# Optimization experiments

Hardware: AMD Instinct MI355X
Metric: run time of the kernel (lower is better)

Reference implementation:

```python
import jax, jax.numpy as jnp
import numpy as np


def setup_inputs() -> dict:
    key = jax.random.key(0)
    ks = jax.random.split(key, 7)
    N, C, sy, sx = 1024, 384, 7, 7
    Dm, Dc = 64, 64
    Dg = C + Dm + Dc  # 512, must match f_t_global
    return {
        "f_t_global": jax.random.normal(ks[0], (N, Dg), dtype=jnp.float32),
        "x_t_local": jax.random.normal(ks[1], (N, C, sy, sx), dtype=jnp.float32),
        "x_t_prev_local": jax.random.normal(ks[2], (N, C, sy, sx), dtype=jnp.float32),
        "m_t": jax.random.normal(ks[3], (N, Dm), dtype=jnp.float32),
        "m_t_prev": jax.random.normal(ks[4], (N, Dm), dtype=jnp.float32),
        "c_t": jax.random.normal(ks[5], (N, Dc), dtype=jnp.float32),
        "c_t_prev": jax.random.normal(ks[6], (N, Dc), dtype=jnp.float32),
    }


def _join(loc, m, c):
    # loc: [S, N, C]; m: [N, Dm]; c: [N, Dc] -> [S, N, C+Dm+Dc]
    S, N, _ = loc.shape
    mc = jnp.concatenate([m, c], axis=-1)  # [N, Dm+Dc]
    mc = jnp.broadcast_to(mc[None], (S, N, mc.shape[-1]))
    return jnp.concatenate([loc, mc], axis=-1)


def _mean_ce_diag(logits):
    # logits: [S, N, N]; labels = arange(N) for every s -> mean over s of CE
    logp = jax.nn.log_softmax(logits, axis=-1)
    diag = jnp.diagonal(logp, axis1=1, axis2=2)  # [S, N]
    return -jnp.mean(diag)  # mean over N (per-step CE) and over S (the /(sx*sy))


def reference(f_t_global, x_t_local, x_t_prev_local, m_t, m_t_prev, c_t, c_t_prev):
    N, C, sy, sx = x_t_prev_local.shape
    S = sy * sx
    # [N,C,sy,sx] -> [S,N,C] (spatial locations batched)
    prev = x_t_prev_local.reshape(N, C, S).transpose(2, 0, 1)
    cur = x_t_local.reshape(N, C, S).transpose(2, 0, 1)
    pos = _join(prev, m_t_prev, c_t_prev)   # [S, N, D]
    # loss1: global features vs per-location previous positives
    logits1 = jnp.einsum('id,sjd->sij', f_t_global, pos)  # [S, N, N]
    loss1 = _mean_ce_diag(logits1)
    # loss2: per-location current predictions vs previous positives
    pred2 = _join(cur, m_t, c_t)            # [S, N, D]
    logits2 = jnp.einsum('sid,sjd->sij', pred2, pos)
    loss2 = _mean_ce_diag(logits2)
    loss = loss1 + loss2
    return (loss, x_t_prev_local, x_t_local)
```

## Files before the change

### kernel.cpp

```cpp
#include <hip/hip_runtime.h>
#include <hip/hip_bf16.h>

typedef __attribute__((ext_vector_type(8))) __bf16 bf16x8;
typedef __attribute__((ext_vector_type(4))) float  f32x4;

#define SDIM 49
#define NDIM 1024
#define CDIM 384
#define DDIM 512
#define DMC  64
#define SCALE (1.0f/(SDIM*NDIM))
#define SLOT 65536

__device__ __forceinline__ void gload16(const void* g, void* l) {
    __builtin_amdgcn_global_load_lds((const __attribute__((address_space(1))) void*)g,
                                     (__attribute__((address_space(3))) void*)l, 16, 0, 0);
}

__global__ __launch_bounds__(512) void pack_copy_kernel(
    const float* __restrict__ xloc, const float* __restrict__ mv,
    const float* __restrict__ cv,   __hip_bfloat16* __restrict__ dst,
    float* __restrict__ cpy)
{
    const int j = blockIdx.x;
    const int d = threadIdx.x;
    float vals[SDIM];
    if (d < CDIM) {
        const float* p = xloc + ((size_t)j * CDIM + d) * SDIM;
        #pragma unroll
        for (int s = 0; s < SDIM; ++s) vals[s] = p[s];
    } else if (d < CDIM + DMC) {
        float v = mv[j * DMC + (d - CDIM)];
        #pragma unroll
        for (int s = 0; s < SDIM; ++s) vals[s] = v;
    } else {
        float v = cv[j * DMC + (d - CDIM - DMC)];
        #pragma unroll
        for (int s = 0; s < SDIM; ++s) vals[s] = v;
    }
    #pragma unroll
    for (int s = 0; s < SDIM; ++s)
        dst[((size_t)s * NDIM + j) * DDIM + d] = __float2bfloat16(vals[s]);

    const float* src = xloc + (size_t)j * CDIM * SDIM;
    float* dcp = cpy + (size_t)j * CDIM * SDIM;
    for (int i = threadIdx.x; i < CDIM * SDIM; i += 512) dcp[i] = src[i];
}

__global__ void fpack_kernel(const float* __restrict__ f,
                             __hip_bfloat16* __restrict__ dst, int n)
{
    int i = blockIdx.x * blockDim.x + threadIdx.x;
    if (i < n) dst[i] = __float2bfloat16(f[i]);
}

__global__ __launch_bounds__(512, 2) void loss_kernel(
    const __hip_bfloat16* __restrict__ Fm,
    const __hip_bfloat16* __restrict__ Km,
    const __hip_bfloat16* __restrict__ Qm,
    float2* __restrict__ part,
    float* __restrict__ out)
{
    extern __shared__ __attribute__((aligned(16))) char sm[];

    const int bid = blockIdx.x;
    const int gid = (bid & 7) * 196 + (bid >> 3);
    const int s   = gid >> 5;
    const int rem = gid & 31;
    const int kb  = rem >> 3;
    const int qb  = rem & 7;

    const int tid  = threadIdx.x;
    const int lane = tid & 63;
    const int w    = tid >> 6;
    const int l15  = lane & 15;
    const int l4   = lane >> 4;
    const int wk   = w >> 2;
    const int wq   = w & 3;

    const char* Ag = (const char*)Km + ((size_t)s * NDIM + (size_t)kb * 256) * 1024;
    const char* Bg = (qb < 4)
        ? ((const char*)Fm + (size_t)qb * 256 * 1024)
        : ((const char*)Qm + ((size_t)s * NDIM + (size_t)(qb - 4) * 256) * 1024);

    const int trow = tid >> 3;
    const int scol = (((tid & 7) ^ ((tid >> 3) & 7)) << 4);

    #define STAGE(T) do {                                                     \
        char* sb_ = sm + (size_t)((T) & 1) * SLOT;                            \
        const size_t ko_ = (size_t)(T) * 128;                                 \
        _Pragma("unroll")                                                     \
        for (int c = 0; c < 4; ++c) {                                         \
            gload16(Ag + (size_t)(c * 64 + trow) * 1024 + ko_ + scol,         \
                    sb_ + c * 8192 + tid * 16);                               \
            gload16(Bg + (size_t)(c * 64 + trow) * 1024 + ko_ + scol,         \
                    sb_ + 32768 + c * 8192 + tid * 16);                       \
        }                                                                     \
    } while (0)

    const unsigned xo   = (unsigned)((l15 & 7) << 4);
    const unsigned arow = (unsigned)((wk * 128 + l15) * 128);
    const unsigned brow = 32768u + (unsigned)((wq * 64 + l15) * 128);

    f32x4 acc[8][4];
    #pragma unroll
    for (int a = 0; a < 8; ++a)
        #pragma unroll
        for (int b = 0; b < 4; ++b) acc[a][b] = f32x4{0.f, 0.f, 0.f, 0.f};

    #define COMPUTE(T) do {                                                   \
        const char* sb_ = sm + (size_t)((T) & 1) * SLOT;                      \
        _Pragma("unroll")                                                     \
        for (int kc = 0; kc < 2; ++kc) {                                      \
            const unsigned col = ((unsigned)(kc * 64 + l4 * 16)) ^ xo;        \
            bf16x8 bfr[4], afr[8];                                            \
            _Pragma("unroll")                                                 \
            for (int b = 0; b < 4; ++b)                                       \
                bfr[b] = *(const bf16x8*)(sb_ + brow + b * 2048 + col);       \
            _Pragma("unroll")                                                 \
            for (int a = 0; a < 8; ++a)                                       \
                afr[a] = *(const bf16x8*)(sb_ + arow + a * 2048 + col);       \
            _Pragma("unroll")                                                 \
            for (int a = 0; a < 8; ++a)                                       \
                _Pragma("unroll")                                             \
                for (int b = 0; b < 4; ++b)                                   \
                    acc[a][b] = __builtin_amdgcn_mfma_f32_16x16x32_bf16(      \
                        afr[a], bfr[b], acc[a][b], 0, 0, 0);                  \
        }                                                                     \
    } while (0)

    STAGE(0);
    for (int t = 0; t < 8; ++t) {
        if (t < 7) {
            STAGE(t + 1);
            asm volatile("s_waitcnt vmcnt(8)" ::: "memory");
        } else {
            asm volatile("s_waitcnt vmcnt(0)" ::: "memory");
        }
        __builtin_amdgcn_s_barrier();
        __builtin_amdgcn_s_setprio(1);
        COMPUTE(t);
        __builtin_amdgcn_s_setprio(0);
        asm volatile("" ::: "memory");
        __builtin_amdgcn_s_barrier();
    }

    float q_m[4], q_s[4];
    #pragma unroll
    for (int b = 0; b < 4; ++b) {
        float m = -3.0e38f;
        #pragma unroll
        for (int a = 0; a < 8; ++a)
            #pragma unroll
            for (int r = 0; r < 4; ++r) m = fmaxf(m, acc[a][b][r]);
        float ss = 0.0f;
        #pragma unroll
        for (int a = 0; a < 8; ++a)
            #pragma unroll
            for (int r = 0; r < 4; ++r) ss += __expf(acc[a][b][r] - m);
        #pragma unroll
        for (int off = 16; off <= 32; off <<= 1) {
            float mo = __shfl_xor(m, off, 64);
            float so = __shfl_xor(ss, off, 64);
            float nm = fmaxf(m, mo);
            ss = ss * __expf(m - nm) + so * __expf(mo - nm);
            m = nm;
        }
        q_m[b] = m; q_s[b] = ss;
    }
    if (lane < 16) {
        const size_t rowb = (size_t)s * 2048 + (size_t)qb * 256 + wq * 64 + lane;
        #pragma unroll
        for (int b = 0; b < 4; ++b)
            part[(rowb + b * 16) * 8 + kb * 2 + wk] = make_float2(q_m[b], q_s[b]);
    }

    if (kb == (qb & 3) && (wq >> 1) == wk) {
        float d = 0.0f;
        const bool lok = (((lane >> 2) & 3) == l4);
        if (wq & 1) {
            #pragma unroll
            for (int b = 0; b < 4; ++b)
                #pragma unroll
                for (int r = 0; r < 4; ++r)
                    if (lok && r == (lane & 3)) d += acc[4 + b][b][r];
        } else {
            #pragma unroll
            for (int b = 0; b < 4; ++b)
                #pragma unroll
                for (int r = 0; r < 4; ++r)
                    if (lok && r == (lane & 3)) d += acc[b][b][r];
        }
        #pragma unroll
        for (int off = 1; off < 64; off <<= 1) d += __shfl_xor(d, off, 64);
        if (lane == 0) atomicAdd(out, -d * SCALE);
    }
    #undef STAGE
    #undef COMPUTE
}

__global__ __launch_bounds__(256) void reduce_kernel(
    const float2* __restrict__ part, float* __restrict__ out)
{
    const int row = blockIdx.x * 256 + threadIdx.x;
    const float2* p = part + (size_t)row * 8;
    float m = -3.0e38f;
    float2 q[8];
    #pragma unroll
    for (int i = 0; i < 8; ++i) { q[i] = p[i]; m = fmaxf(m, q[i].x); }
    float ssum = 0.0f;
    #pragma unroll
    for (int i = 0; i < 8; ++i) ssum += q[i].y * __expf(q[i].x - m);
    float v = m + __logf(ssum);
    #pragma unroll
    for (int off = 1; off < 64; off <<= 1) v += __shfl_xor(v, off, 64);
    __shared__ float red[4];
    const int lane = threadIdx.x & 63, w = threadIdx.x >> 6;
    if (lane == 0) red[w] = v;
    __syncthreads();
    if (threadIdx.x == 0)
        atomicAdd(out, (red[0] + red[1] + red[2] + red[3]) * SCALE);
}

extern "C" void kernel_launch(void* const* d_in, const int* in_sizes, int n_in,
                              void* d_out, int out_size, void* d_ws, size_t ws_size,
                              hipStream_t stream)
{
    (void)in_sizes; (void)n_in; (void)out_size; (void)ws_size;
    const float* f  = (const float*)d_in[0];
    const float* x  = (const float*)d_in[1];
    const float* xp = (const float*)d_in[2];
    const float* mt = (const float*)d_in[3];
    const float* mp = (const float*)d_in[4];
    const float* ct = (const float*)d_in[5];
    const float* cp = (const float*)d_in[6];
    float* out = (float*)d_out;

    char* ws = (char*)d_ws;
    const size_t packBytes = (size_t)SDIM * NDIM * DDIM * 2;
    __hip_bfloat16* Km = (__hip_bfloat16*)ws;
    __hip_bfloat16* Qm = (__hip_bfloat16*)(ws + packBytes);
    __hip_bfloat16* Fm = (__hip_bfloat16*)(ws + 2 * packBytes);
    float2* part = (float2*)(ws + 2 * packBytes + (size_t)NDIM * DDIM * 2);

    hipMemsetAsync(out, 0, sizeof(float), stream);

    const int sz = NDIM * CDIM * SDIM;
    pack_copy_kernel<<<NDIM, 512, 0, stream>>>(xp, mp, cp, Km, out + 1);
    pack_copy_kernel<<<NDIM, 512, 0, stream>>>(x,  mt, ct, Qm, out + 1 + sz);
    fpack_kernel<<<(NDIM * DDIM + 255) / 256, 256, 0, stream>>>(f, Fm, NDIM * DDIM);

    loss_kernel<<<1568, 512, 2 * SLOT, stream>>>(Fm, Km, Qm, part, out);
    reduce_kernel<<<392, 256, 0, stream>>>(part, out);
}
```

Measured before the change: 255.8 us.

## Split K-step into four quadrant phases interleaving LDS reads, prefetch and MFMA

Restructures the GEMM main loop into a four-phase ping-pong schedule. The LDS fragment reads for A and B halves, the global-to-LDS prefetch halves of the next tile, and the MFMA quadrants are interleaved, with barriers separating each phase. The goal is to overlap LDS traffic and global loads with matrix-core work and to lower register pressure by holding only half the fragments at a time. The extra barriers per iteration (eight instead of two) and the full vmcnt(0) wait inside each step could cost more synchronisation time than the overlap saves.

```diff
diff --git a/kernel.cpp b/kernel.cpp
--- a/kernel.cpp
+++ b/kernel.cpp
@@ -86,15 +86,15 @@
     const int trow = tid >> 3;
     const int scol = (((tid & 7) ^ ((tid >> 3) & 7)) << 4);
 
-    #define STAGE(T) do {                                                     \
-        char* sb_ = sm + (size_t)((T) & 1) * SLOT;                            \
+    #define STAGE_HALF(T, H) do {                                             \
+        char* db_ = sm + (size_t)((T) & 1) * SLOT;                            \
         const size_t ko_ = (size_t)(T) * 128;                                 \
         _Pragma("unroll")                                                     \
-        for (int c = 0; c < 4; ++c) {                                         \
+        for (int c = 2 * (H); c < 2 * (H) + 2; ++c) {                         \
             gload16(Ag + (size_t)(c * 64 + trow) * 1024 + ko_ + scol,         \
-                    sb_ + c * 8192 + tid * 16);                               \
+                    db_ + c * 8192 + tid * 16);                               \
             gload16(Bg + (size_t)(c * 64 + trow) * 1024 + ko_ + scol,         \
-                    sb_ + 32768 + c * 8192 + tid * 16);                       \
+                    db_ + 32768 + c * 8192 + tid * 16);                       \
         }                                                                     \
     } while (0)
 
@@ -108,40 +108,67 @@
         #pragma unroll
         for (int b = 0; b < 4; ++b) acc[a][b] = f32x4{0.f, 0.f, 0.f, 0.f};
 
-    #define COMPUTE(T) do {                                                   \
-        const char* sb_ = sm + (size_t)((T) & 1) * SLOT;                      \
-        _Pragma("unroll")                                                     \
-        for (int kc = 0; kc < 2; ++kc) {                                      \
-            const unsigned col = ((unsigned)(kc * 64 + l4 * 16)) ^ xo;        \
-            bf16x8 bfr[4], afr[8];                                            \
+    bf16x8 afr[4][2], bfr[4][2];
+
+    #define READ_A(H) do {                                                    \
+        _Pragma("unroll")                                                     \
+        for (int a = 0; a < 4; ++a)                                           \
             _Pragma("unroll")                                                 \
-            for (int b = 0; b < 4; ++b)                                       \
-                bfr[b] = *(const bf16x8*)(sb_ + brow + b * 2048 + col);       \
+            for (int kc = 0; kc < 2; ++kc)                                    \
+                afr[a][kc] = *(const bf16x8*)(sb_ + arow + (H) * 8192u        \
+                    + a * 2048u + (((unsigned)(kc * 64 + l4 * 16)) ^ xo));    \
+    } while (0)
+
+    #define READ_B(H) do {                                                    \
+        _Pragma("unroll")                                                     \
+        for (int b = 0; b < 2; ++b)                                           \
             _Pragma("unroll")                                                 \
-            for (int a = 0; a < 8; ++a)                                       \
-                afr[a] = *(const bf16x8*)(sb_ + arow + a * 2048 + col);       \
+            for (int kc = 0; kc < 2; ++kc)                                    \
+                bfr[(H)*2 + b][kc] = *(const bf16x8*)(sb_ + brow              \
+                    + ((H)*2 + b) * 2048u                                     \
+                    + (((unsigned)(kc * 64 + l4 * 16)) ^ xo));                \
+    } while (0)
+
+    #define MFMA_Q(AH, BH) do {                                               \
+        _Pragma("unroll")                                                     \
+        for (int a = 0; a < 4; ++a)                                           \
             _Pragma("unroll")                                                 \
-            for (int a = 0; a < 8; ++a)                                       \
+            for (int b = 0; b < 2; ++b)                                       \
                 _Pragma("unroll")                                             \
-                for (int b = 0; b < 4; ++b)                                   \
-                    acc[a][b] = __builtin_amdgcn_mfma_f32_16x16x32_bf16(      \
-                        afr[a], bfr[b], acc[a][b], 0, 0, 0);                  \
-        }                                                                     \
-    } while (0)
-
-    STAGE(0);
+                for (int kc = 0; kc < 2; ++kc)                                \
+                    acc[(AH)*4 + a][(BH)*2 + b] =                             \
+                        __builtin_amdgcn_mfma_f32_16x16x32_bf16(              \
+                            afr[a][kc], bfr[(BH)*2 + b][kc],                  \
+                            acc[(AH)*4 + a][(BH)*2 + b], 0, 0, 0);            \
+    } while (0)
+
+    STAGE_HALF(0, 0); STAGE_HALF(0, 1);
+    asm volatile("s_waitcnt vmcnt(0)" ::: "memory");
+    __builtin_amdgcn_s_barrier();
+
     for (int t = 0; t < 8; ++t) {
-        if (t < 7) {
-            STAGE(t + 1);
-            asm volatile("s_waitcnt vmcnt(8)" ::: "memory");
-        } else {
-            asm volatile("s_waitcnt vmcnt(0)" ::: "memory");
-        }
-        __builtin_amdgcn_s_barrier();
-        __builtin_amdgcn_s_setprio(1);
-        COMPUTE(t);
-        __builtin_amdgcn_s_setprio(0);
-        asm volatile("" ::: "memory");
+        const char* sb_ = sm + (size_t)(t & 1) * SLOT;
+        const bool pf = (t < 7);
+        READ_A(0); READ_B(0);
+        if (pf) STAGE_HALF(t + 1, 0);
+        __builtin_amdgcn_s_barrier();
+        asm volatile("s_waitcnt lgkmcnt(0)" ::: "memory");
+        __builtin_amdgcn_s_setprio(1); MFMA_Q(0, 0); __builtin_amdgcn_s_setprio(0);
+        __builtin_amdgcn_s_barrier();
+        READ_B(1);
+        if (pf) STAGE_HALF(t + 1, 1);
+        __builtin_amdgcn_s_barrier();
+        asm volatile("s_waitcnt lgkmcnt(0)" ::: "memory");
+        __builtin_amdgcn_s_setprio(1); MFMA_Q(0, 1); __builtin_amdgcn_s_setprio(0);
+        __builtin_amdgcn_s_barrier();
+        READ_A(1);
+        __builtin_amdgcn_s_barrier();
+        asm volatile("s_waitcnt lgkmcnt(0)" ::: "memory");
+        __builtin_amdgcn_s_setprio(1); MFMA_Q(1, 0); __builtin_amdgcn_s_setprio(0);
+        __builtin_amdgcn_s_barrier();
+        asm volatile("s_waitcnt vmcnt(0)" ::: "memory");
+        __builtin_amdgcn_s_barrier();
+        __builtin_amdgcn_s_setprio(1); MFMA_Q(1, 1); __builtin_amdgcn_s_setprio(0);
         __builtin_amdgcn_s_barrier();
     }
 
@@ -195,8 +222,10 @@
         for (int off = 1; off < 64; off <<= 1) d += __shfl_xor(d, off, 64);
         if (lane == 0) atomicAdd(out, -d * SCALE);
     }
-    #undef STAGE
-    #undef COMPUTE
+    #undef STAGE_HALF
+    #undef READ_A
+    #undef READ_B
+    #undef MFMA_Q
 }
 
 __global__ __launch_bounds__(256) void reduce_kernel(
```

New measurement: 252.5 us. No clear change (-1.3%).

## Make loss kernel persistent with 256x128 tiles and 32x32 MFMA

Applied to the files above, without the earlier changes.

Replaces the 1568-block loss GEMM grid, which used 256x256 tiles and 16x16x32 MFMAs, with a persistent 256-block kernel. Each block walks 392/32 tile groups of 256x128 using 32x32x16 bf16 MFMAs and prefetches the next tile's first K-slice across tile boundaries. It also folds the output copy of x into the per-thread pack loop rather than running a separate strided copy. The goal is to cut launch and tail overhead and raise MFMA efficiency. The costs are lower per-CU occupancy (256 threads, one block) and a wait for all loads before each step.

```diff
diff --git a/kernel.cpp b/kernel.cpp
--- a/kernel.cpp
+++ b/kernel.cpp
@@ -1,8 +1,8 @@
 #include <hip/hip_runtime.h>
 #include <hip/hip_bf16.h>
 
-typedef __attribute__((ext_vector_type(8))) __bf16 bf16x8;
-typedef __attribute__((ext_vector_type(4))) float  f32x4;
+typedef __attribute__((ext_vector_type(8)))  __bf16 bf16x8;
+typedef __attribute__((ext_vector_type(16))) float  f32x16;
 
 #define SDIM 49
 #define NDIM 1024
@@ -10,7 +10,7 @@
 #define DDIM 512
 #define DMC  64
 #define SCALE (1.0f/(SDIM*NDIM))
-#define SLOT 65536
+#define PSLOT 49152
 
 __device__ __forceinline__ void gload16(const void* g, void* l) {
     __builtin_amdgcn_global_load_lds((const __attribute__((address_space(1))) void*)g,
@@ -29,6 +29,9 @@
         const float* p = xloc + ((size_t)j * CDIM + d) * SDIM;
         #pragma unroll
         for (int s = 0; s < SDIM; ++s) vals[s] = p[s];
+        float* dcp = cpy + ((size_t)j * CDIM + d) * SDIM;
+        #pragma unroll
+        for (int s = 0; s < SDIM; ++s) dcp[s] = vals[s];
     } else if (d < CDIM + DMC) {
         float v = mv[j * DMC + (d - CDIM)];
         #pragma unroll
@@ -41,10 +44,6 @@
     #pragma unroll
     for (int s = 0; s < SDIM; ++s)
         dst[((size_t)s * NDIM + j) * DDIM + d] = __float2bfloat16(vals[s]);
-
-    const float* src = xloc + (size_t)j * CDIM * SDIM;
-    float* dcp = cpy + (size_t)j * CDIM * SDIM;
-    for (int i = threadIdx.x; i < CDIM * SDIM; i += 512) dcp[i] = src[i];
 }
 
 __global__ void fpack_kernel(const float* __restrict__ f,
@@ -54,7 +53,7 @@
     if (i < n) dst[i] = __float2bfloat16(f[i]);
 }
 
-__global__ __launch_bounds__(512, 2) void loss_kernel(
+__global__ __launch_bounds__(256, 1) void loss_kernel(
     const __hip_bfloat16* __restrict__ Fm,
     const __hip_bfloat16* __restrict__ Km,
     const __hip_bfloat16* __restrict__ Qm,
@@ -64,139 +63,158 @@
     extern __shared__ __attribute__((aligned(16))) char sm[];
 
     const int bid = blockIdx.x;
-    const int gid = (bid & 7) * 196 + (bid >> 3);
-    const int s   = gid >> 5;
-    const int rem = gid & 31;
-    const int kb  = rem >> 3;
-    const int qb  = rem & 7;
+    const int xcd = bid & 7;
+    const int jj  = bid >> 3;
 
     const int tid  = threadIdx.x;
     const int lane = tid & 63;
-    const int w    = tid >> 6;
-    const int l15  = lane & 15;
-    const int l4   = lane >> 4;
-    const int wk   = w >> 2;
-    const int wq   = w & 3;
-
-    const char* Ag = (const char*)Km + ((size_t)s * NDIM + (size_t)kb * 256) * 1024;
-    const char* Bg = (qb < 4)
-        ? ((const char*)Fm + (size_t)qb * 256 * 1024)
-        : ((const char*)Qm + ((size_t)s * NDIM + (size_t)(qb - 4) * 256) * 1024);
-
-    const int trow = tid >> 3;
-    const int scol = (((tid & 7) ^ ((tid >> 3) & 7)) << 4);
-
-    #define STAGE(T) do {                                                     \
-        char* sb_ = sm + (size_t)((T) & 1) * SLOT;                            \
-        const size_t ko_ = (size_t)(T) * 128;                                 \
-        _Pragma("unroll")                                                     \
-        for (int c = 0; c < 4; ++c) {                                         \
-            gload16(Ag + (size_t)(c * 64 + trow) * 1024 + ko_ + scol,         \
-                    sb_ + c * 8192 + tid * 16);                               \
-            gload16(Bg + (size_t)(c * 64 + trow) * 1024 + ko_ + scol,         \
-                    sb_ + 32768 + c * 8192 + tid * 16);                       \
-        }                                                                     \
-    } while (0)
-
-    const unsigned xo   = (unsigned)((l15 & 7) << 4);
-    const unsigned arow = (unsigned)((wk * 128 + l15) * 128);
-    const unsigned brow = 32768u + (unsigned)((wq * 64 + l15) * 128);
-
-    f32x4 acc[8][4];
-    #pragma unroll
-    for (int a = 0; a < 8; ++a)
-        #pragma unroll
-        for (int b = 0; b < 4; ++b) acc[a][b] = f32x4{0.f, 0.f, 0.f, 0.f};
-
-    #define COMPUTE(T) do {                                                   \
-        const char* sb_ = sm + (size_t)((T) & 1) * SLOT;                      \
-        _Pragma("unroll")                                                     \
-        for (int kc = 0; kc < 2; ++kc) {                                      \
-            const unsigned col = ((unsigned)(kc * 64 + l4 * 16)) ^ xo;        \
-            bf16x8 bfr[4], afr[8];                                            \
-            _Pragma("unroll")                                                 \
-            for (int b = 0; b < 4; ++b)                                       \
-                bfr[b] = *(const bf16x8*)(sb_ + brow + b * 2048 + col);       \
-            _Pragma("unroll")                                                 \
-            for (int a = 0; a < 8; ++a)                                       \
-                afr[a] = *(const bf16x8*)(sb_ + arow + a * 2048 + col);       \
-            _Pragma("unroll")                                                 \
-            for (int a = 0; a < 8; ++a)                                       \
-                _Pragma("unroll")                                             \
-                for (int b = 0; b < 4; ++b)                                   \
-                    acc[a][b] = __builtin_amdgcn_mfma_f32_16x16x32_bf16(      \
-                        afr[a], bfr[b], acc[a][b], 0, 0, 0);                  \
-        }                                                                     \
-    } while (0)
-
-    STAGE(0);
-    for (int t = 0; t < 8; ++t) {
-        if (t < 7) {
-            STAGE(t + 1);
-            asm volatile("s_waitcnt vmcnt(8)" ::: "memory");
-        } else {
+    const int wv   = tid >> 6;
+    const int r31  = lane & 31;
+    const int hi   = lane >> 5;
+    const int wk   = wv >> 1;
+    const int wq   = wv & 1;
+
+    const int srccol = (((lane & 7) ^ (lane >> 3)) << 4);
+    const int lrow   = lane >> 3;
+
+    auto APtr = [&](int g) -> const char* {
+        const int s = g >> 6, kb = (g >> 4) & 3;
+        return (const char*)Km + ((size_t)s * NDIM + (size_t)kb * 256) * 1024;
+    };
+    auto BPtr = [&](int g) -> const char* {
+        const int s = g >> 6, qb = g & 15;
+        return (qb < 8)
+            ? ((const char*)Fm + (size_t)qb * 128 * 1024)
+            : ((const char*)Qm + ((size_t)s * NDIM + (size_t)(qb - 8) * 128) * 1024);
+    };
+    auto stage12 = [&](const char* A, const char* B, int ko, char* slot) {
+        #pragma unroll
+        for (int k = 0; k < 8; ++k) {
+            const int ch = wv + 4 * k;
+            gload16(A + (size_t)(ch * 8 + lrow) * 1024 + ko + srccol,
+                    slot + ch * 1024 + lane * 16);
+        }
+        #pragma unroll
+        for (int k = 0; k < 4; ++k) {
+            const int ch = wv + 4 * k;
+            gload16(B + (size_t)(ch * 8 + lrow) * 1024 + ko + srccol,
+                    slot + 32768 + ch * 1024 + lane * 16);
+        }
+    };
+
+    const unsigned xo    = (unsigned)((r31 & 7) << 4);
+    const unsigned abase = (unsigned)((wk * 128 + r31) * 128);
+    const unsigned bbase = 32768u + (unsigned)((wq * 64 + r31) * 128);
+
+    f32x16 acc[4][2];
+    bf16x8 af[4][4], bf[2][4];
+
+    {
+        const int g0 = xcd * 392 + jj;
+        stage12(APtr(g0), BPtr(g0), 0, sm);
+    }
+
+    for (int l = jj; l < 392; l += 32) {
+        const int g = xcd * 392 + l;
+        const char* Ag = APtr(g);
+        const char* Bg = BPtr(g);
+        const bool hasNext = (l + 32) < 392;
+        const int gn = hasNext ? (g + 32) : g;
+        const char* An = APtr(gn);
+        const char* Bn = BPtr(gn);
+
+        #pragma unroll
+        for (int ka = 0; ka < 4; ++ka)
+            #pragma unroll
+            for (int qc = 0; qc < 2; ++qc) acc[ka][qc] = f32x16{};
+
+        #pragma unroll
+        for (int t = 0; t < 8; ++t) {
+            const char* sb_ = sm + (size_t)(t & 1) * PSLOT;
+            char* ns_ = sm + (size_t)((t + 1) & 1) * PSLOT;
+            const bool pf = (t < 7) || hasNext;
+
             asm volatile("s_waitcnt vmcnt(0)" ::: "memory");
-        }
-        __builtin_amdgcn_s_barrier();
-        __builtin_amdgcn_s_setprio(1);
-        COMPUTE(t);
-        __builtin_amdgcn_s_setprio(0);
-        asm volatile("" ::: "memory");
-        __builtin_amdgcn_s_barrier();
+            __builtin_amdgcn_s_barrier();
+
+            if (pf) {
+                if (t < 7) stage12(Ag, Bg, (t + 1) * 128, ns_);
+                else       stage12(An, Bn, 0, ns_);
+            }
+
+            #pragma unroll
+            for (int kc = 0; kc < 4; ++kc) {
+                const unsigned co = ((unsigned)(kc * 32 + hi * 16)) ^ xo;
+                #pragma unroll
+                for (int ka = 0; ka < 4; ++ka)
+                    af[ka][kc] = *(const bf16x8*)(sb_ + abase + ka * 4096u + co);
+                #pragma unroll
+                for (int qc = 0; qc < 2; ++qc)
+                    bf[qc][kc] = *(const bf16x8*)(sb_ + bbase + qc * 4096u + co);
+            }
+            __builtin_amdgcn_s_setprio(1);
+            #pragma unroll
+            for (int kc = 0; kc < 4; ++kc)
+                #pragma unroll
+                for (int ka = 0; ka < 4; ++ka)
+                    #pragma unroll
+                    for (int qc = 0; qc < 2; ++qc)
+                        acc[ka][qc] = __builtin_amdgcn_mfma_f32_32x32x16_bf16(
+                            af[ka][kc], bf[qc][kc], acc[ka][qc], 0, 0, 0);
+            __builtin_amdgcn_s_setprio(0);
+        }
+
+        const int s  = g >> 6;
+        const int kb = (g >> 4) & 3;
+        const int qb = g & 15;
+
+        #pragma unroll
+        for (int qc = 0; qc < 2; ++qc) {
+            float m = -3.0e38f;
+            #pragma unroll
+            for (int ka = 0; ka < 4; ++ka)
+                #pragma unroll
+                for (int r = 0; r < 16; ++r) m = fmaxf(m, acc[ka][qc][r]);
+            float ss = 0.0f;
+            #pragma unroll
+            for (int ka = 0; ka < 4; ++ka)
+                #pragma unroll
+                for (int r = 0; r < 16; ++r) ss += __expf(acc[ka][qc][r] - m);
+            {
+                float mo = __shfl_xor(m, 32, 64), so = __shfl_xor(ss, 32, 64);
+                float nm = fmaxf(m, mo);
+                ss = ss * __expf(m - nm) + so * __expf(mo - nm); m = nm;
+            }
+            if (!hi) {
+                const size_t row = (size_t)s * 2048 + (size_t)qb * 128
+                                 + wq * 64 + qc * 32 + r31;
+                part[row * 8 + kb * 2 + wk] = make_float2(m, ss);
+            }
+        }
+
+        if ((qb & 7) == kb * 2 + wk) {
+            const int regd = (r31 & 3) | ((r31 >> 3) << 2);
+            float d = 0.0f;
+            if (hi == ((r31 >> 2) & 1)) {
+                if (wq) {
+                    #pragma unroll
+                    for (int qc = 0; qc < 2; ++qc)
+                        #pragma unroll
+                        for (int r = 0; r < 16; ++r)
+                            if (r == regd) d += acc[2 + qc][qc][r];
+                } else {
+                    #pragma unroll
+                    for (int qc = 0; qc < 2; ++qc)
+                        #pragma unroll
+                        for (int r = 0; r < 16; ++r)
+                            if (r == regd) d += acc[qc][qc][r];
+                }
+            }
+            #pragma unroll
+            for (int off = 1; off < 64; off <<= 1) d += __shfl_xor(d, off, 64);
+            if (lane == 0) atomicAdd(out, -d * SCALE);
+        }
     }
-
-    float q_m[4], q_s[4];
-    #pragma unroll
-    for (int b = 0; b < 4; ++b) {
-        float m = -3.0e38f;
-        #pragma unroll
-        for (int a = 0; a < 8; ++a)
-            #pragma unroll
-            for (int r = 0; r < 4; ++r) m = fmaxf(m, acc[a][b][r]);
-        float ss = 0.0f;
-        #pragma unroll
-        for (int a = 0; a < 8; ++a)
-            #pragma unroll
-            for (int r = 0; r < 4; ++r) ss += __expf(acc[a][b][r] - m);
-        #pragma unroll
-        for (int off = 16; off <= 32; off <<= 1) {
-            float mo = __shfl_xor(m, off, 64);
-            float so = __shfl_xor(ss, off, 64);
-            float nm = fmaxf(m, mo);
-            ss = ss * __expf(m - nm) + so * __expf(mo - nm);
-            m = nm;
-        }
-        q_m[b] = m; q_s[b] = ss;
-    }
-    if (lane < 16) {
-        const size_t rowb = (size_t)s * 2048 + (size_t)qb * 256 + wq * 64 + lane;
-        #pragma unroll
-        for (int b = 0; b < 4; ++b)
-            part[(rowb + b * 16) * 8 + kb * 2 + wk] = make_float2(q_m[b], q_s[b]);
-    }
-
-    if (kb == (qb & 3) && (wq >> 1) == wk) {
-        float d = 0.0f;
-        const bool lok = (((lane >> 2) & 3) == l4);
-        if (wq & 1) {
-            #pragma unroll
-            for (int b = 0; b < 4; ++b)
-                #pragma unroll
-                for (int r = 0; r < 4; ++r)
-                    if (lok && r == (lane & 3)) d += acc[4 + b][b][r];
-        } else {
-            #pragma unroll
-            for (int b = 0; b < 4; ++b)
-                #pragma unroll
-                for (int r = 0; r < 4; ++r)
-                    if (lok && r == (lane & 3)) d += acc[b][b][r];
-        }
-        #pragma unroll
-        for (int off = 1; off < 64; off <<= 1) d += __shfl_xor(d, off, 64);
-        if (lane == 0) atomicAdd(out, -d * SCALE);
-    }
-    #undef STAGE
-    #undef COMPUTE
 }
 
 __global__ __launch_bounds__(256) void reduce_kernel(
@@ -250,6 +268,6 @@
     pack_copy_kernel<<<NDIM, 512, 0, stream>>>(x,  mt, ct, Qm, out + 1 + sz);
     fpack_kernel<<<(NDIM * DDIM + 255) / 256, 256, 0, stream>>>(f, Fm, NDIM * DDIM);
 
-    loss_kernel<<<1568, 512, 2 * SLOT, stream>>>(Fm, Km, Qm, part, out);
+    loss_kernel<<<256, 256, 2 * PSLOT, stream>>>(Fm, Km, Qm, part, out);
     reduce_kernel<<<392, 256, 0, stream>>>(part, out);
 }
```

After: 272.2 us. 6.4% more time.
